# Performance work log

Hardware: AMD Instinct MI355X
Metric: run time of the kernel (lower is better)

Reference implementation:

```python
import jax, jax.numpy as jnp
import numpy as np

# Module hyperparameters (from init_kwargs)
IOU_T = 0.5
PROB_T = 0.75
COV = 10.0
TOPK = 500       # self.topk
PRE_K = 2048     # fixed-shape cap on post-threshold candidates entering NMS
B, C, H, W = 4, 4, 160, 160


def setup_inputs() -> dict:
    key = jax.random.key(0)
    k1, k2 = jax.random.split(key)
    mask = jax.random.normal(k1, (B, C, H, W), dtype=jnp.float32)
    # scale bias so boxes have ~10px extent (realistic detections)
    bias = jax.random.normal(k2, (B, 4, H, W), dtype=jnp.float32) * 8.0
    return {"mask": mask, "bias": bias}


def _pos_grid(h, w):
    # equivalent of np.dstack(np.mgrid[0:h, 0:w]) -> [h, w, 2] with (y, x)
    yy, xx = jnp.meshgrid(jnp.arange(h), jnp.arange(w), indexing="ij")
    return jnp.stack([yy, xx], axis=-1).astype(jnp.float32)


def _pairwise_iou(b):
    # b: [K, 4] as (y1, x1, y2, x2); torchvision-style IoU (areas unclamped, inter clamped)
    area = (b[:, 2] - b[:, 0]) * (b[:, 3] - b[:, 1])
    lt = jnp.maximum(b[:, None, :2], b[None, :, :2])
    rb = jnp.minimum(b[:, None, 2:], b[None, :, 2:])
    wh = jnp.clip(rb - lt, 0.0)
    inter = wh[..., 0] * wh[..., 1]
    return inter / (area[:, None] + area[None, :] - inter)


def _nms_keep(iou, valid, thresh):
    # boxes are pre-sorted by descending score; greedy suppression
    K = iou.shape[0]
    idx = jnp.arange(K)
    def body(i, keep):
        sup = (iou[i] > thresh) & (idx > i) & keep[i]
        return keep & ~sup
    return jax.lax.fori_loop(0, K, body, valid)


def _per_image(mask_i, bias_i, pos):
    # mask_i: [C, h, w], bias_i: [4, h, w], pos: [h, w, 2]
    p = jax.nn.softmax(mask_i, axis=0)
    prob = jax.lax.stop_gradient(p.max(axis=0))          # prob.detach()
    cls = p.argmax(axis=0)
    frontal = (cls != 0) & (prob > PROB_T)               # [h, w]
    # boxes = pos tiled to (y,x,y,x) + bias.permute(0,2,3,1)
    boxes = jnp.concatenate([pos, pos], axis=-1) + jnp.transpose(bias_i, (1, 2, 0))
    boxes = boxes.reshape(-1, 4)                          # [h*w, 4]
    score = jnp.where(frontal.reshape(-1), prob.reshape(-1), -1.0)
    # fixed-size candidate set, sorted by descending score (invalid -> -1)
    top_s, idx = jax.lax.top_k(score, PRE_K)
    cand = boxes[idx]
    valid = top_s > 0.0                                   # valid scores > PROB_T > 0
    keep = _nms_keep(_pairwise_iou(cand), valid, IOU_T)
    kept_s = jnp.where(keep, top_s, -1.0)
    fin_s, fi = jax.lax.top_k(kept_s, TOPK)               # min(topk, n) via padding
    fboxes = cand[fi]                                     # [TOPK, 4]
    fvalid = fin_s > 0.0
    fprob = jnp.where(fvalid, fin_s, 0.0)
    mu = (fboxes[:, :2] + fboxes[:, 2:]) * 0.5            # [TOPK, 2]
    sigma = fboxes[:, 2:] - fboxes[:, :2]
    sigma = jnp.where(fvalid[:, None], sigma, 1.0)        # safe divisor for padding
    # gaussian2d: z = (pos - mu) / (sigma / cov); heat = max_n exp(-|z|^2/2) * prob
    z = (pos[None] - mu[:, None, None, :]) / (sigma[:, None, None, :] / COV)  # [TOPK,h,w,2]
    g = jnp.exp(-0.5 * (z ** 2).sum(axis=-1)) * fprob[:, None, None]
    heat = g.max(axis=0)                                  # [h, w]; all-padded -> 0, matches n==0 case
    return heat, fboxes, fvalid


def reference(mask, bias):
    pos = _pos_grid(mask.shape[2], mask.shape[3])
    heat, fboxes, fvalid = jax.vmap(lambda m, b: _per_image(m, b, pos))(mask, bias)
    # original returns (heatmaps, mask, boxes); boxes padded to [B, TOPK, 4] with validity mask
    return heat, mask, fboxes, fvalid
```

## Files before the change

### kernel.cpp

```cpp
#include <hip/hip_runtime.h>
#include <math.h>

#define BATCH 4
#define NCH 4
#define H 160
#define W 160
#define NPIX (H * W)
#define NTILE (NPIX / 256)
#define PRE_K 2048
#define TOPK 500
#define PROB_T 0.75f
#define IOU_T 0.5f
#define COV 10.0f

#define SCORE_OFF 0u
#define KEY_OFF   409600u
#define F_OFF     1228800u
#define CSC_OFF   1261632u
#define CBOX_OFF  1294400u
#define SUP_OFF   1425472u
#define NV_OFF    3523648u
#define PAR_OFF   3523712u
#define FLAG_OFF  3563712u
#define BCNT_OFF  3571904u

#define OUT_HEAT_OFF 0
#define OUT_MASK_OFF 102400
#define OUT_BOX_OFF  512000
#define OUT_VAL_OFF  520000

typedef unsigned long long u64;
typedef unsigned int u32;

__device__ __forceinline__ int block_scan_excl(int v, int tid, int* tmp, int* total) {
    tmp[tid] = v;
    __syncthreads();
    for (int off = 1; off < 256; off <<= 1) {
        int y = (tid >= off) ? tmp[tid - off] : 0;
        __syncthreads();
        tmp[tid] += y;
        __syncthreads();
    }
    int incl = tmp[tid];
    *total = tmp[255];
    __syncthreads();
    return incl - v;
}

__global__ void k_score(const float* __restrict__ mask, float* __restrict__ score,
                        float* __restrict__ out_mask, int* __restrict__ blkcnt) {
    int b = blockIdx.y;
    int pix = blockIdx.x * 256 + threadIdx.x;
    const float* mp = mask + (size_t)b * NCH * NPIX + pix;
    float* op = out_mask + (size_t)b * NCH * NPIX + pix;
    float x0 = mp[0], x1 = mp[NPIX], x2 = mp[2 * NPIX], x3 = mp[3 * NPIX];
    op[0] = x0; op[NPIX] = x1; op[2 * NPIX] = x2; op[3 * NPIX] = x3;
    float m = x0; int c = 0;
    if (x1 > m) { m = x1; c = 1; }
    if (x2 > m) { m = x2; c = 2; }
    if (x3 > m) { m = x3; c = 3; }
    float sum = ((expf(x0 - m) + expf(x1 - m)) + expf(x2 - m)) + expf(x3 - m);
    float prob = 1.0f / sum;
    bool frontal = (c != 0) && (prob > PROB_T);
    score[(size_t)b * NPIX + pix] = frontal ? prob : -1.0f;
    __shared__ int wcnt[4];
    u64 bm = __ballot(frontal);
    if ((threadIdx.x & 63) == 0) wcnt[threadIdx.x >> 6] = __popcll(bm);
    __syncthreads();
    if (threadIdx.x == 0)
        blkcnt[b * NTILE + blockIdx.x] = wcnt[0] + wcnt[1] + wcnt[2] + wcnt[3];
}

__global__ void __launch_bounds__(256)
k_compact(const float* __restrict__ score, const float* __restrict__ bias,
          const int* __restrict__ blkcnt, u64* __restrict__ keys,
          int* __restrict__ Fout, float* __restrict__ cand_score,
          float* __restrict__ cand_box) {
    int b = blockIdx.y;
    int bx = blockIdx.x;
    int tid = threadIdx.x;
    const int* bc = blkcnt + b * NTILE;
    int f_base = 0, F = 0;
    #pragma unroll 4
    for (int k = 0; k < NTILE; ++k) {
        int c = bc[k];
        F += c;
        if (k < bx) f_base += c;
    }
    int pix = bx * 256 + tid;
    float s = score[(size_t)b * NPIX + pix];
    bool fr = (s > 0.0f);
    int lane = tid & 63, wv = tid >> 6;
    int v = fr ? 1 : 0;
    int incl = v;
    for (int off = 1; off < 64; off <<= 1) {
        int y = __shfl_up(incl, off);
        if (lane >= off) incl += y;
    }
    __shared__ int wtot[4];
    __shared__ int wpre[4];
    if (lane == 63) wtot[wv] = incl;
    __syncthreads();
    if (tid == 0) {
        int acc = 0;
        for (int k = 0; k < 4; ++k) { wpre[k] = acc; acc += wtot[k]; }
    }
    __syncthreads();
    int f_local = wpre[wv] + (incl - v);
    if (fr) {
        u32 lo = 0x7FFFFFFFu - (u32)pix;
        keys[(size_t)b * NPIX + f_base + f_local] =
            ((u64)__float_as_uint(s) << 32) | (u64)lo;
    }
    if (bx == 0 && tid == 0) Fout[b] = F;
    if (!fr) {
        int nf_base = bx * 256 - f_base;
        int nf_local = tid - f_local;
        int slot = F + nf_base + nf_local;
        if (slot < PRE_K) {
            const float* bb = bias + (size_t)b * 4 * NPIX;
            cand_score[(size_t)b * PRE_K + slot] = -1.0f;
            float y = (float)(pix / W), x = (float)(pix % W);
            float4 box;
            box.x = y + bb[0 * NPIX + pix];
            box.y = x + bb[1 * NPIX + pix];
            box.z = y + bb[2 * NPIX + pix];
            box.w = x + bb[3 * NPIX + pix];
            ((float4*)cand_box)[(size_t)b * PRE_K + slot] = box;
        }
    }
}

#define RK_CH 4096
__global__ void k_rank(const u64* __restrict__ keys, const float* __restrict__ bias,
                       const int* __restrict__ Fout, float* __restrict__ cand_score,
                       float* __restrict__ cand_box) {
    int b = blockIdx.y;
    int F = Fout[b];
    if (blockIdx.x * 256 >= F) return;
    int i = blockIdx.x * 256 + threadIdx.x;
    const u64* kb = keys + (size_t)b * NPIX;
    u64 ki = (i < F) ? kb[i] : 0;
    int rank = 0;
    __shared__ u64 ks[RK_CH];
    for (int base = 0; base < F; base += RK_CH) {
        int lim = min(RK_CH, F - base);
        __syncthreads();
        for (int k = threadIdx.x; k < lim; k += 256) ks[k] = kb[base + k];
        __syncthreads();
        if (i < F) {
            int k = 0;
            for (; k + 8 <= lim; k += 8) {
                rank += (ks[k]     > ki) ? 1 : 0;
                rank += (ks[k + 1] > ki) ? 1 : 0;
                rank += (ks[k + 2] > ki) ? 1 : 0;
                rank += (ks[k + 3] > ki) ? 1 : 0;
                rank += (ks[k + 4] > ki) ? 1 : 0;
                rank += (ks[k + 5] > ki) ? 1 : 0;
                rank += (ks[k + 6] > ki) ? 1 : 0;
                rank += (ks[k + 7] > ki) ? 1 : 0;
            }
            for (; k < lim; ++k) rank += (ks[k] > ki) ? 1 : 0;
        }
    }
    if (i < F && rank < PRE_K) {
        float si = __uint_as_float((u32)(ki >> 32));
        int xi = 0x7FFFFFFF - (int)(u32)(ki & 0xFFFFFFFFu);
        cand_score[(size_t)b * PRE_K + rank] = si;
        const float* bb = bias + (size_t)b * 4 * NPIX;
        float y = (float)(xi / W), x = (float)(xi % W);
        float4 box;
        box.x = y + bb[0 * NPIX + xi];
        box.y = x + bb[1 * NPIX + xi];
        box.z = y + bb[2 * NPIX + xi];
        box.w = x + bb[3 * NPIX + xi];
        ((float4*)cand_box)[(size_t)b * PRE_K + rank] = box;
    }
}

__global__ void __launch_bounds__(512)
k_iou(const float* __restrict__ cand_box, const int* __restrict__ Fout,
      u32* __restrict__ sup, unsigned char* __restrict__ flag) {
    int b = blockIdx.y;
    int F = Fout[b];
    int V = F < PRE_K ? F : PRE_K;
    int r0 = blockIdx.x * 8;
    if (r0 >= V) return;
    __shared__ float ly1[PRE_K], lx1[PRE_K], ly2[PRE_K], lx2[PRE_K], lar[PRE_K];
    for (int k = threadIdx.x; k < PRE_K; k += 512) {
        float4 v = ((const float4*)cand_box)[(size_t)b * PRE_K + k];
        ly1[k] = v.x; lx1[k] = v.y; ly2[k] = v.z; lx2[k] = v.w;
        lar[k] = (v.z - v.x) * (v.w - v.y);
    }
    __syncthreads();
    int lr = threadIdx.x >> 6;
    int w = threadIdx.x & 63;
    int i = r0 + lr;
    float ay1 = ly1[i], ax1 = lx1[i], ay2 = ly2[i], ax2 = lx2[i], aa = lar[i];
    u32 bits = 0;
    int jbase = w * 32;
    #pragma unroll 4
    for (int jj = 0; jj < 32; ++jj) {
        int jo = (jj + w) & 31;
        int j = jbase + jo;
        if (j > i) {
            float lty = fmaxf(ay1, ly1[j]);
            float ltx = fmaxf(ax1, lx1[j]);
            float rby = fminf(ay2, ly2[j]);
            float rbx = fminf(ax2, lx2[j]);
            float wy = fmaxf(rby - lty, 0.0f);
            float wx = fmaxf(rbx - ltx, 0.0f);
            float inter = wy * wx;
            float iou = inter / ((aa + lar[j]) - inter);
            if (iou > IOU_T) bits |= (1u << jo);
        }
    }
    sup[((size_t)b * PRE_K + i) * 64 + w] = bits;
    bool any = __any(bits != 0u);
    if (w == 0) flag[(size_t)b * PRE_K + i] = any ? 1 : 0;
}

__global__ void __launch_bounds__(256)
k_nmsfin(const u32* __restrict__ sup, const unsigned char* __restrict__ flag,
         const int* __restrict__ Fout, const float* __restrict__ cand_score,
         const float* __restrict__ cand_box, float* __restrict__ out_boxes,
         float* __restrict__ out_valid, float* __restrict__ params,
         int* __restrict__ NV) {
    int b = blockIdx.x;
    int tid = threadIdx.x;
    int F = Fout[b];
    int V = F < PRE_K ? F : PRE_K;
    __shared__ int rid_s[PRE_K];
    __shared__ int M_s;
    __shared__ u32 kws[64];
    __shared__ int tmp[256];

    if (tid < 64) {
        int lane = tid;
        const u32* f32 = (const u32*)(flag + (size_t)b * PRE_K);
        u32 fw[8];
        #pragma unroll
        for (int k = 0; k < 8; ++k) fw[k] = f32[lane * 8 + k];
        int r0 = lane * 32;
        int cnt = 0;
        #pragma unroll
        for (int k = 0; k < 8; ++k)
            #pragma unroll
            for (int j = 0; j < 4; ++j) {
                int r = r0 + k * 4 + j;
                if (((fw[k] >> (8 * j)) & 0xFFu) != 0u && r < V) ++cnt;
            }
        int incl = cnt;
        for (int off = 1; off < 64; off <<= 1) {
            int y = __shfl_up(incl, off);
            if (lane >= off) incl += y;
        }
        if (lane == 63) M_s = incl;
        int pos = incl - cnt;
        #pragma unroll
        for (int k = 0; k < 8; ++k)
            #pragma unroll
            for (int j = 0; j < 4; ++j) {
                int r = r0 + k * 4 + j;
                if (((fw[k] >> (8 * j)) & 0xFFu) != 0u && r < V) rid_s[pos++] = r;
            }
    }
    __syncthreads();

    if (tid < 64) {
        int lane = tid;
        int M = M_s;
        int rem = V - lane * 32;
        u32 kw = (rem >= 32) ? 0xFFFFFFFFu : (rem <= 0 ? 0u : ((1u << rem) - 1u));
        const u32* supb = sup + (size_t)b * PRE_K * 64 + lane;
        int C = (M + 7) >> 3;
        int C4 = (C + 3) & ~3;
        int l7 = lane & 7;
        u32 rbuf[4][8];
        int ridv[4];

        #define LOAD_RID(slot, c) ridv[slot] = rid_s[min((c) * 8 + l7, PRE_K - 1)]
        #define ISSUE(slot) do { \
            _Pragma("unroll") \
            for (int k_ = 0; k_ < 8; ++k_) { \
                int i_ = __builtin_amdgcn_readlane(ridv[slot], k_) & (PRE_K - 1); \
                rbuf[slot][k_] = supb[(size_t)i_ * 64]; \
            } \
        } while (0)
        #define PROC(slot, c) do { \
            _Pragma("unroll") \
            for (int k_ = 0; k_ < 8; ++k_) { \
                int m_ = (c) * 8 + k_; \
                if (m_ < M) { \
                    int i_ = __builtin_amdgcn_readlane(ridv[slot], k_) & (PRE_K - 1); \
                    u32 kb_ = (u32)__builtin_amdgcn_readlane((int)kw, i_ >> 5); \
                    if ((kb_ >> (i_ & 31)) & 1u) kw &= ~rbuf[slot][k_]; \
                } \
            } \
        } while (0)

        LOAD_RID(0, 0); LOAD_RID(1, 1); LOAD_RID(2, 2); LOAD_RID(3, 3);
        ISSUE(0); ISSUE(1); ISSUE(2);
        for (int c = 0; c < C4; c += 4) {
            PROC(0, c);     ISSUE(3);            LOAD_RID(0, c + 4);
            PROC(1, c + 1); ISSUE(0);            LOAD_RID(1, c + 5);
            PROC(2, c + 2); ISSUE(1);            LOAD_RID(2, c + 6);
            PROC(3, c + 3); ISSUE(2);            LOAD_RID(3, c + 7);
        }
        #undef LOAD_RID
        #undef ISSUE
        #undef PROC
        kws[lane] = kw;
    }
    __syncthreads();

    int s0 = tid * 8;
    int bits8 = (int)((kws[s0 >> 5] >> (s0 & 31)) & 0xFFu);
    int cnt = __popc(bits8);
    int tot;
    int kpre = block_scan_excl(cnt, tid, tmp, &tot);
    int NK = tot;
    for (int k = 0; k < 8; ++k) {
        int s = s0 + k;
        int kept = (bits8 >> k) & 1;
        int pos = kept ? kpre : (NK + s - kpre);
        if (pos < TOPK) {
            float4 bx = ((const float4*)cand_box)[(size_t)b * PRE_K + s];
            ((float4*)out_boxes)[(size_t)b * TOPK + pos] = bx;
            out_valid[(size_t)b * TOPK + pos] = kept ? 1.0f : 0.0f;
            if (kept) {
                float scv = cand_score[(size_t)b * PRE_K + s];
                float* pp = params + ((size_t)b * TOPK + pos) * 5;
                pp[0] = (bx.x + bx.z) * 0.5f;
                pp[1] = (bx.y + bx.w) * 0.5f;
                pp[2] = (bx.z - bx.x) / COV;
                pp[3] = (bx.w - bx.y) / COV;
                pp[4] = scv;
            }
        }
        kpre += kept;
    }
    if (tid == 0) NV[b] = NK < TOPK ? NK : TOPK;
}

#define TILE 16
#define TPL (W / TILE)
__global__ void k_heat(const float* __restrict__ params, const int* __restrict__ NV,
                       float* __restrict__ heat) {
    int b = blockIdx.y;
    int ty0 = (blockIdx.x / TPL) * TILE;
    int tx0 = (blockIdx.x % TPL) * TILE;
    int tid = threadIdx.x;
    int nv = NV[b];
    __shared__ float lp[TOPK * 5];
    __shared__ int cntS;
    if (tid == 0) cntS = 0;
    __syncthreads();
    for (int t = tid; t < nv; t += 256) {
        const float* pp = params + ((size_t)b * TOPK + t) * 5;
        float muy = pp[0], mux = pp[1], dy = pp[2], dx = pp[3], p = pp[4];
        float cy = fmaxf(fmaxf((float)ty0 - muy, muy - (float)(ty0 + TILE - 1)), 0.0f);
        float cx = fmaxf(fmaxf((float)tx0 - mux, mux - (float)(tx0 + TILE - 1)), 0.0f);
        float zy = cy / fabsf(dy);
        float zx = cx / fabsf(dx);
        float z2 = zy * zy + zx * zx;
        if (!(z2 > 40.0f)) {
            int idx = atomicAdd(&cntS, 1);
            float* q = lp + idx * 5;
            q[0] = muy; q[1] = mux; q[2] = dy; q[3] = dx; q[4] = p;
        }
    }
    __syncthreads();
    int n = cntS;
    float py = (float)(ty0 + (tid >> 4));
    float px = (float)(tx0 + (tid & 15));
    float m = 0.0f;
    for (int t = 0; t < n; ++t) {
        float muy = lp[t * 5 + 0], mux = lp[t * 5 + 1];
        float dy = lp[t * 5 + 2], dx = lp[t * 5 + 3], p = lp[t * 5 + 4];
        float zy = (py - muy) / dy;
        float zx = (px - mux) / dx;
        float g = expf(-0.5f * (zy * zy + zx * zx)) * p;
        m = fmaxf(m, g);
    }
    heat[(size_t)b * NPIX + (ty0 + (tid >> 4)) * W + tx0 + (tid & 15)] = m;
}

extern "C" void kernel_launch(void* const* d_in, const int* in_sizes, int n_in,
                              void* d_out, int out_size, void* d_ws, size_t ws_size,
                              hipStream_t stream) {
    const float* mask = (const float*)d_in[0];
    const float* bias = (const float*)d_in[1];
    float* out = (float*)d_out;
    char* ws = (char*)d_ws;

    float* score      = (float*)(ws + SCORE_OFF);
    u64*   keys       = (u64*)(ws + KEY_OFF);
    int*   Fout       = (int*)(ws + F_OFF);
    float* cand_score = (float*)(ws + CSC_OFF);
    float* cand_box   = (float*)(ws + CBOX_OFF);
    u32*   sup        = (u32*)(ws + SUP_OFF);
    int*   NV         = (int*)(ws + NV_OFF);
    float* params     = (float*)(ws + PAR_OFF);
    unsigned char* flag = (unsigned char*)(ws + FLAG_OFF);
    int*   blkcnt     = (int*)(ws + BCNT_OFF);

    dim3 g100(NTILE, BATCH);
    k_score<<<g100, 256, 0, stream>>>(mask, score, out + OUT_MASK_OFF, blkcnt);
    k_compact<<<g100, 256, 0, stream>>>(score, bias, blkcnt, keys, Fout,
                                        cand_score, cand_box);
    k_rank<<<g100, 256, 0, stream>>>(keys, bias, Fout, cand_score, cand_box);
    k_iou<<<dim3(PRE_K / 8, BATCH), 512, 0, stream>>>(cand_box, Fout, sup, flag);
    k_nmsfin<<<BATCH, 256, 0, stream>>>(sup, flag, Fout, cand_score, cand_box,
                                        out + OUT_BOX_OFF, out + OUT_VAL_OFF, params, NV);
    k_heat<<<dim3(TPL * (H / TILE), BATCH), 256, 0, stream>>>(params, NV, out + OUT_HEAT_OFF);
}
```

Baseline: 115.5 us.

## Fuse compaction and ranking into one kernel with per-wave full-array rank counting

The score kernel now writes packed 64-bit (score, pixel) keys directly, with zero for non-frontal pixels, so the separate float score buffer goes away. The old compact and rank kernels are merged into one. Each block compacts its frontal keys into shared memory and fills the padding slots. Each wave then ranks one item by scanning all per-image keys in global memory and reducing the count with shuffles. This saves a kernel launch and a scatter pass, but every frontal item now compares against all pixels instead of only the frontal set, and those reads come from global memory instead of shared memory.

```diff
diff --git a/kernel.cpp b/kernel.cpp
--- a/kernel.cpp
+++ b/kernel.cpp
@@ -13,16 +13,15 @@
 #define IOU_T 0.5f
 #define COV 10.0f
 
-#define SCORE_OFF 0u
-#define KEY_OFF   409600u
-#define F_OFF     1228800u
-#define CSC_OFF   1261632u
-#define CBOX_OFF  1294400u
-#define SUP_OFF   1425472u
-#define NV_OFF    3523648u
-#define PAR_OFF   3523712u
-#define FLAG_OFF  3563712u
-#define BCNT_OFF  3571904u
+#define KEY_OFF   0u
+#define F_OFF     819200u
+#define CSC_OFF   819264u
+#define CBOX_OFF  852032u
+#define SUP_OFF   983104u
+#define NV_OFF    3080256u
+#define PAR_OFF   3080320u
+#define FLAG_OFF  3120320u
+#define BCNT_OFF  3128512u
 
 #define OUT_HEAT_OFF 0
 #define OUT_MASK_OFF 102400
@@ -47,7 +46,7 @@
     return incl - v;
 }
 
-__global__ void k_score(const float* __restrict__ mask, float* __restrict__ score,
+__global__ void k_score(const float* __restrict__ mask, u64* __restrict__ keys,
                         float* __restrict__ out_mask, int* __restrict__ blkcnt) {
     int b = blockIdx.y;
     int pix = blockIdx.x * 256 + threadIdx.x;
@@ -62,7 +61,10 @@
     float sum = ((expf(x0 - m) + expf(x1 - m)) + expf(x2 - m)) + expf(x3 - m);
     float prob = 1.0f / sum;
     bool frontal = (c != 0) && (prob > PROB_T);
-    score[(size_t)b * NPIX + pix] = frontal ? prob : -1.0f;
+    u64 key = frontal
+        ? (((u64)__float_as_uint(prob) << 32) | (u64)(0x7FFFFFFFu - (u32)pix))
+        : 0ull;
+    keys[(size_t)b * NPIX + pix] = key;
     __shared__ int wcnt[4];
     u64 bm = __ballot(frontal);
     if ((threadIdx.x & 63) == 0) wcnt[threadIdx.x >> 6] = __popcll(bm);
@@ -72,53 +74,46 @@
 }
 
 __global__ void __launch_bounds__(256)
-k_compact(const float* __restrict__ score, const float* __restrict__ bias,
-          const int* __restrict__ blkcnt, u64* __restrict__ keys,
-          int* __restrict__ Fout, float* __restrict__ cand_score,
-          float* __restrict__ cand_box) {
+k_rankpad(const u64* __restrict__ keys, const float* __restrict__ bias,
+          const int* __restrict__ blkcnt, int* __restrict__ Fout,
+          float* __restrict__ cand_score, float* __restrict__ cand_box) {
     int b = blockIdx.y;
     int bx = blockIdx.x;
     int tid = threadIdx.x;
+    int lane = tid & 63, wv = tid >> 6;
     const int* bc = blkcnt + b * NTILE;
-    int f_base = 0, F = 0;
+    const float* bb = bias + (size_t)b * 4 * NPIX;
+    int F = 0, f_base = 0;
     #pragma unroll 4
     for (int k = 0; k < NTILE; ++k) {
         int c = bc[k];
         F += c;
         if (k < bx) f_base += c;
     }
+    if (bx == 0 && tid == 0) Fout[b] = F;
     int pix = bx * 256 + tid;
-    float s = score[(size_t)b * NPIX + pix];
-    bool fr = (s > 0.0f);
-    int lane = tid & 63, wv = tid >> 6;
-    int v = fr ? 1 : 0;
-    int incl = v;
+    u64 myk = keys[(size_t)b * NPIX + pix];
+    int fr = (myk != 0ull) ? 1 : 0;
+    int incl = fr;
     for (int off = 1; off < 64; off <<= 1) {
         int y = __shfl_up(incl, off);
         if (lane >= off) incl += y;
     }
-    __shared__ int wtot[4];
-    __shared__ int wpre[4];
+    __shared__ int wtot[4], wpre[5];
+    __shared__ u64 items[256];
     if (lane == 63) wtot[wv] = incl;
     __syncthreads();
     if (tid == 0) {
         int acc = 0;
         for (int k = 0; k < 4; ++k) { wpre[k] = acc; acc += wtot[k]; }
-    }
-    __syncthreads();
-    int f_local = wpre[wv] + (incl - v);
-    if (fr) {
-        u32 lo = 0x7FFFFFFFu - (u32)pix;
-        keys[(size_t)b * NPIX + f_base + f_local] =
-            ((u64)__float_as_uint(s) << 32) | (u64)lo;
-    }
-    if (bx == 0 && tid == 0) Fout[b] = F;
-    if (!fr) {
-        int nf_base = bx * 256 - f_base;
-        int nf_local = tid - f_local;
-        int slot = F + nf_base + nf_local;
+        wpre[4] = acc;
+    }
+    __syncthreads();
+    int f_local = wpre[wv] + (incl - fr);
+    if (fr) items[f_local] = myk;
+    if (!fr && F < PRE_K) {
+        int slot = F + (pix - f_base - f_local);
         if (slot < PRE_K) {
-            const float* bb = bias + (size_t)b * 4 * NPIX;
             cand_score[(size_t)b * PRE_K + slot] = -1.0f;
             float y = (float)(pix / W), x = (float)(pix % W);
             float4 box;
@@ -129,52 +124,32 @@
             ((float4*)cand_box)[(size_t)b * PRE_K + slot] = box;
         }
     }
-}
-
-#define RK_CH 4096
-__global__ void k_rank(const u64* __restrict__ keys, const float* __restrict__ bias,
-                       const int* __restrict__ Fout, float* __restrict__ cand_score,
-                       float* __restrict__ cand_box) {
-    int b = blockIdx.y;
-    int F = Fout[b];
-    if (blockIdx.x * 256 >= F) return;
-    int i = blockIdx.x * 256 + threadIdx.x;
+    __syncthreads();
+    int nI = wpre[4];
     const u64* kb = keys + (size_t)b * NPIX;
-    u64 ki = (i < F) ? kb[i] : 0;
-    int rank = 0;
-    __shared__ u64 ks[RK_CH];
-    for (int base = 0; base < F; base += RK_CH) {
-        int lim = min(RK_CH, F - base);
-        __syncthreads();
-        for (int k = threadIdx.x; k < lim; k += 256) ks[k] = kb[base + k];
-        __syncthreads();
-        if (i < F) {
-            int k = 0;
-            for (; k + 8 <= lim; k += 8) {
-                rank += (ks[k]     > ki) ? 1 : 0;
-                rank += (ks[k + 1] > ki) ? 1 : 0;
-                rank += (ks[k + 2] > ki) ? 1 : 0;
-                rank += (ks[k + 3] > ki) ? 1 : 0;
-                rank += (ks[k + 4] > ki) ? 1 : 0;
-                rank += (ks[k + 5] > ki) ? 1 : 0;
-                rank += (ks[k + 6] > ki) ? 1 : 0;
-                rank += (ks[k + 7] > ki) ? 1 : 0;
-            }
-            for (; k < lim; ++k) rank += (ks[k] > ki) ? 1 : 0;
-        }
-    }
-    if (i < F && rank < PRE_K) {
-        float si = __uint_as_float((u32)(ki >> 32));
-        int xi = 0x7FFFFFFF - (int)(u32)(ki & 0xFFFFFFFFu);
-        cand_score[(size_t)b * PRE_K + rank] = si;
-        const float* bb = bias + (size_t)b * 4 * NPIX;
-        float y = (float)(xi / W), x = (float)(xi % W);
-        float4 box;
-        box.x = y + bb[0 * NPIX + xi];
-        box.y = x + bb[1 * NPIX + xi];
-        box.z = y + bb[2 * NPIX + xi];
-        box.w = x + bb[3 * NPIX + xi];
-        ((float4*)cand_box)[(size_t)b * PRE_K + rank] = box;
+    for (int it = wv; it < nI; it += 4) {
+        u64 ki = items[it];
+        int cnt = 0;
+        for (int j0 = 0; j0 < NPIX; j0 += 256) {
+            cnt += (kb[j0 + lane]       > ki) ? 1 : 0;
+            cnt += (kb[j0 + 64 + lane]  > ki) ? 1 : 0;
+            cnt += (kb[j0 + 128 + lane] > ki) ? 1 : 0;
+            cnt += (kb[j0 + 192 + lane] > ki) ? 1 : 0;
+        }
+        for (int off = 32; off > 0; off >>= 1) cnt += __shfl_down(cnt, off);
+        if (lane == 0 && cnt < PRE_K) {
+            int rank = cnt;
+            float si = __uint_as_float((u32)(ki >> 32));
+            int xi = 0x7FFFFFFF - (int)(u32)(ki & 0xFFFFFFFFu);
+            cand_score[(size_t)b * PRE_K + rank] = si;
+            float y = (float)(xi / W), x = (float)(xi % W);
+            float4 box;
+            box.x = y + bb[0 * NPIX + xi];
+            box.y = x + bb[1 * NPIX + xi];
+            box.z = y + bb[2 * NPIX + xi];
+            box.w = x + bb[3 * NPIX + xi];
+            ((float4*)cand_box)[(size_t)b * PRE_K + rank] = box;
+        }
     }
 }
 
@@ -394,7 +369,6 @@
     float* out = (float*)d_out;
     char* ws = (char*)d_ws;
 
-    float* score      = (float*)(ws + SCORE_OFF);
     u64*   keys       = (u64*)(ws + KEY_OFF);
     int*   Fout       = (int*)(ws + F_OFF);
     float* cand_score = (float*)(ws + CSC_OFF);
@@ -406,12 +380,10 @@
     int*   blkcnt     = (int*)(ws + BCNT_OFF);
 
     dim3 g100(NTILE, BATCH);
-    k_score<<<g100, 256, 0, stream>>>(mask, score, out + OUT_MASK_OFF, blkcnt);
-    k_compact<<<g100, 256, 0, stream>>>(score, bias, blkcnt, keys, Fout,
-                                        cand_score, cand_box);
-    k_rank<<<g100, 256, 0, stream>>>(keys, bias, Fout, cand_score, cand_box);
+    k_score<<<g100, 256, 0, stream>>>(mask, keys, out + OUT_MASK_OFF, blkcnt);
+    k_rankpad<<<g100, 256, 0, stream>>>(keys, bias, blkcnt, Fout, cand_score, cand_box);
     k_iou<<<dim3(PRE_K / 8, BATCH), 512, 0, stream>>>(cand_box, Fout, sup, flag);
     k_nmsfin<<<BATCH, 256, 0, stream>>>(sup, flag, Fout, cand_score, cand_box,
                                         out + OUT_BOX_OFF, out + OUT_VAL_OFF, params, NV);
-    k_heat<<<dim3(TPL * (H / TILE), BATCH), 256, 0, stream>>>(params, NV, out + OUT_HEAT_OFF);
-}
+    k_heat<<<g100, 256, 0, stream>>>(params, NV, out + OUT_HEAT_OFF);
+}
```

New measurement: 199.4 us. 72.7% more time.
